# Optimization experiments

Measured on AMD Instinct MI355X. Metric: run time of the kernel, lower is better.

## Reference

```python
import jax, jax.numpy as jnp
import numpy as np

B, S, D = 16, 2048, 128


def setup_inputs() -> dict:
    key = jax.random.key(0)
    kq, kk, kv, km = jax.random.split(key, 4)
    q = jax.random.normal(kq, (B, S, D), dtype=jnp.float32)
    k = jax.random.normal(kk, (B, S, D), dtype=jnp.float32)
    v = jax.random.normal(kv, (B, S, D), dtype=jnp.float32)
    mask = jax.random.randint(km, (B, S, S), 0, 2, dtype=jnp.int32)
    return {"q": q, "k": k, "v": v, "mask": mask}


def softmax_one(x):
    # repo's softmax_one: subtract max, denominator is 1 + sum(exp)
    x = x - jnp.max(x, axis=-1, keepdims=True)
    e = jnp.exp(x)
    return e / (1.0 + jnp.sum(e, axis=-1, keepdims=True))


def reference(q, k, v, mask):
    d_k = k.shape[-1]
    zero = jnp.zeros((q.shape[0], 1, d_k), dtype=q.dtype)
    # prepend zero 'sink' key/value token along the sequence axis
    k1 = jnp.concatenate([zero, k], axis=1)          # [B, S+1, D]
    v1 = jnp.concatenate([zero, v], axis=1)          # [B, S+1, D]
    scores = jnp.einsum('bqd,bkd->bqk', q, k1) / np.sqrt(d_k)  # [B, S, S+1]
    # F.pad(mask, (1, 0)) pads sink column with 0 -> sink score masked
    m = jnp.pad(mask, ((0, 0), (0, 0), (1, 0)))
    scores = jnp.where(m == 0, jnp.float32(-1e9), scores)
    p_attn = softmax_one(scores)                     # [B, S, S+1]
    out = jnp.einsum('bqk,bkd->bqd', p_attn, v1)     # [B, S, D]
    return (out, p_attn)
```

## Files before the change

### kernel.cpp

```cpp
#include <hip/hip_runtime.h>
#include <hip/hip_bf16.h>

typedef __attribute__((ext_vector_type(8))) __bf16 bf16x8;
typedef __attribute__((ext_vector_type(4))) __bf16 bf16x4;
typedef __attribute__((ext_vector_type(4))) float  f32x4;
typedef float f32x4u __attribute__((ext_vector_type(4), aligned(4)));

#define NB 16
#define NS 2048
#define ND 128
#define QT 64
#define KT 64
#define NKT (NS / KT)
#define SCALE 0.08838834764831845f

__device__ __forceinline__ bf16x8 ld8_256(const __bf16* base, int row, int byteInRow) {
    int off = row * 256 + (byteInRow ^ ((row & 7) << 4));
    return *reinterpret_cast<const bf16x8*>(reinterpret_cast<const char*>(base) + off);
}
__device__ __forceinline__ bf16x8 ld8_128(const __bf16* base, int row, int byteInRow) {
    int off = row * 128 + (byteInRow ^ ((row & 7) << 4));
    return *reinterpret_cast<const bf16x8*>(reinterpret_cast<const char*>(base) + off);
}
__device__ __forceinline__ void glds16(const void* g, void* l) {
    __builtin_amdgcn_global_load_lds(
        (const __attribute__((address_space(1))) unsigned int*)g,
        (__attribute__((address_space(3))) unsigned int*)l, 16, 0, 0);
}

__global__ __launch_bounds__(256) void conv_qk(const float* __restrict__ q,
                                               const float* __restrict__ k,
                                               __bf16* __restrict__ qb,
                                               __bf16* __restrict__ kb) {
    size_t i = (size_t)blockIdx.x * 256 + threadIdx.x;
    const float4* qs = (const float4*)q;
    const float4* ks = (const float4*)k;
    float4 a = qs[2 * i], b = qs[2 * i + 1];
    bf16x8 o;
    o[0] = (__bf16)(a.x * SCALE); o[1] = (__bf16)(a.y * SCALE);
    o[2] = (__bf16)(a.z * SCALE); o[3] = (__bf16)(a.w * SCALE);
    o[4] = (__bf16)(b.x * SCALE); o[5] = (__bf16)(b.y * SCALE);
    o[6] = (__bf16)(b.z * SCALE); o[7] = (__bf16)(b.w * SCALE);
    *(bf16x8*)&qb[i * 8] = o;
    a = ks[2 * i]; b = ks[2 * i + 1];
    o[0] = (__bf16)a.x; o[1] = (__bf16)a.y; o[2] = (__bf16)a.z; o[3] = (__bf16)a.w;
    o[4] = (__bf16)b.x; o[5] = (__bf16)b.y; o[6] = (__bf16)b.z; o[7] = (__bf16)b.w;
    *(bf16x8*)&kb[i * 8] = o;
}

__global__ __launch_bounds__(256) void conv_vt(const float* __restrict__ v,
                                               __bf16* __restrict__ vt) {
    int b = blockIdx.x >> 4, st = blockIdx.x & 15;
    int s0 = st * 128, t = threadIdx.x;
    #pragma unroll
    for (int i = 0; i < 8; ++i) {
        int task = i * 256 + t;
        int d = task & 127, sg = task >> 7;
        bf16x8 o;
        #pragma unroll
        for (int j = 0; j < 8; ++j)
            o[j] = (__bf16)v[((size_t)b * NS + s0 + sg * 8 + j) * ND + d];
        *(bf16x8*)&vt[((size_t)b * ND + d) * NS + s0 + sg * 8] = o;
    }
}

__global__ __launch_bounds__(256, 2) void qa_main(
    const __bf16* __restrict__ qb, const __bf16* __restrict__ kb,
    const __bf16* __restrict__ vtb, const int* __restrict__ mg,
    float* __restrict__ outg, float* __restrict__ pg)
{
    __shared__ __align__(16) char bufs[3][KT * ND * 2];
    __shared__ unsigned int bm[QT * 68];
    __shared__ __align__(16) __bf16 Ps[4][16 * KT];

    const int bid = blockIdx.x;
    const int lb  = (bid & 7) * 64 + (bid >> 3);
    const int b   = lb >> 5;
    const int q0  = (lb & 31) * QT;
    const int t   = threadIdx.x;
    const int w   = t >> 6;
    const int l   = t & 63;
    const int l15 = l & 15;
    const int g   = l >> 4;

    const __bf16* kbB  = kb  + (size_t)b * NS * ND;
    const __bf16* vtbB = vtb + (size_t)b * ND * NS;

    #pragma unroll 2
    for (int i = 0; i < 32; ++i) {
        int task = i * 2 + (l >> 5);
        (void)task;
        break;
    }
    for (int i = 0; i < 128; ++i) {
        int row = w * 16 + (i >> 3), chunk = i & 7;
        const int4* mp = (const int4*)(mg + (size_t)(b * NS + q0 + row) * NS + chunk * 256) + l;
        int4 mv = *mp;
        unsigned long long b0 = __ballot(mv.x != 0);
        unsigned long long b1 = __ballot(mv.y != 0);
        unsigned long long b2 = __ballot(mv.z != 0);
        unsigned long long b3 = __ballot(mv.w != 0);
        if (l == 0) {
            uint4 lo = { (unsigned)b0, (unsigned)b1, (unsigned)b2, (unsigned)b3 };
            uint4 hi = { (unsigned)(b0 >> 32), (unsigned)(b1 >> 32),
                         (unsigned)(b2 >> 32), (unsigned)(b3 >> 32) };
            *(uint4*)&bm[row * 68 + chunk * 8]     = lo;
            *(uint4*)&bm[row * 68 + chunk * 8 + 4] = hi;
        }
    }

    if (t < QT) pg[(size_t)(b * NS + q0 + t) * (size_t)(NS + 1)] = 0.0f;

    bf16x8 qf[4];
    {
        const __bf16* qrow = qb + (size_t)(b * NS + q0 + w * 16 + l15) * ND;
        #pragma unroll
        for (int kc = 0; kc < 4; ++kc)
            qf[kc] = *(const bf16x8*)(qrow + kc * 32 + g * 8);
    }

    auto stageK = [&](char* buf, int k0) {
        #pragma unroll
        for (int i = 0; i < 4; ++i) {
            int c = i * 256 + t;
            int row = c >> 4, pc = c & 15, lc = pc ^ (row & 7);
            glds16(kbB + (size_t)(k0 + row) * ND + lc * 8, buf + c * 16);
        }
    };
    auto stageV = [&](char* buf, int k0) {
        #pragma unroll
        for (int i = 0; i < 4; ++i) {
            int c = i * 256 + t;
            int d = c >> 3, pc = c & 7, lc = pc ^ (d & 7);
            glds16(vtbB + (size_t)d * NS + k0 + lc * 8, buf + c * 16);
        }
    };

    stageK(bufs[0], 0);
    __syncthreads();

    const int myrow = w * 16 + l15;
    float mrun = -1e9f, srun = 0.0f;

    for (int kt = 0; kt < NKT; ++kt) {
        const int k0 = kt * KT;
        if (kt + 1 < NKT) stageK(bufs[(kt + 1) & 1], k0 + KT);
        const __bf16* Kbuf = (const __bf16*)bufs[kt & 1];

        f32x4 acc[4];
        #pragma unroll
        for (int c = 0; c < 4; ++c) {
            f32x4 z = {0.f, 0.f, 0.f, 0.f}; acc[c] = z;
            #pragma unroll
            for (int kc = 0; kc < 4; ++kc) {
                bf16x8 kf = ld8_256(Kbuf, c * 16 + l15, kc * 64 + g * 16);
                acc[c] = __builtin_amdgcn_mfma_f32_16x16x32_bf16(kf, qf[kc], acc[c], 0, 0, 0);
            }
        }

        uint4 W = *(const uint4*)&bm[myrow * 68 + (k0 >> 8) * 8 + ((k0 & 128) >> 5)];
        unsigned Wr[4] = { W.x, W.y, W.z, W.w };
        const int sh = ((k0 & 64) >> 2) + g;

        float sv[16], tmax = -1e30f;
        #pragma unroll
        for (int c = 0; c < 4; ++c)
            #pragma unroll
            for (int r = 0; r < 4; ++r) {
                float s = ((Wr[r] >> (sh + c * 4)) & 1u) ? acc[c][r] : -1e30f;
                sv[c * 4 + r] = s;
                tmax = fmaxf(tmax, s);
            }
        tmax = fmaxf(tmax, __shfl_xor(tmax, 16));
        tmax = fmaxf(tmax, __shfl_xor(tmax, 32));
        float mnew = fmaxf(mrun, tmax);
        float corr = __expf(mrun - mnew);
        float ps = 0.f;
        #pragma unroll
        for (int i = 0; i < 16; ++i) ps += __expf(sv[i] - mnew);
        ps += __shfl_xor(ps, 16);
        ps += __shfl_xor(ps, 32);
        srun = srun * corr + ps;
        mrun = mnew;
        __syncthreads();
    }

    const float inv = 1.0f / (1.0f + srun);

    f32x4 oacc[8];
    #pragma unroll
    for (int cf = 0; cf < 8; ++cf) { f32x4 z = {0.f,0.f,0.f,0.f}; oacc[cf] = z; }

    stageK(bufs[0], 0);
    stageV(bufs[1], 0);
    __syncthreads();

    int iA = 0, iB = 1, iC = 2;
    const size_t prow = (size_t)(b * NS + q0 + myrow) * (size_t)(NS + 1);
    __bf16* Psw = Ps[w];

    for (int kt = 0; kt < NKT; ++kt) {
        const int k0 = kt * KT;
        if (kt + 1 < NKT) stageK(bufs[iC], k0 + KT);
        const __bf16* Kbuf = (const __bf16*)bufs[iA];

        f32x4 acc[4];
        #pragma unroll
        for (int c = 0; c < 4; ++c) {
            f32x4 z = {0.f, 0.f, 0.f, 0.f}; acc[c] = z;
            #pragma unroll
            for (int kc = 0; kc < 4; ++kc) {
                bf16x8 kf = ld8_256(Kbuf, c * 16 + l15, kc * 64 + g * 16);
                acc[c] = __builtin_amdgcn_mfma_f32_16x16x32_bf16(kf, qf[kc], acc[c], 0, 0, 0);
            }
        }

        uint4 W = *(const uint4*)&bm[myrow * 68 + (k0 >> 8) * 8 + ((k0 & 128) >> 5)];
        unsigned Wr[4] = { W.x, W.y, W.z, W.w };
        const int sh = ((k0 & 64) >> 2) + g;

        #pragma unroll
        for (int c = 0; c < 4; ++c) {
            f32x4 pv;
            bf16x4 pb;
            #pragma unroll
            for (int r = 0; r < 4; ++r) {
                bool on = (Wr[r] >> (sh + c * 4)) & 1u;
                float p = on ? __expf(acc[c][r] - mrun) * inv : 0.0f;
                pv[r] = p;
                pb[r] = (__bf16)p;
            }
            *(f32x4u*)&pg[prow + 1 + k0 + c * 16 + g * 4] = pv;
            int off = l15 * 128 + ((c * 32 + g * 8) ^ ((l15 & 7) << 4));
            *(bf16x4*)((char*)Psw + off) = pb;
        }

        __syncthreads();
        if (kt + 1 < NKT) stageV(bufs[iA], k0 + KT);
        const __bf16* Vbuf = (const __bf16*)bufs[iB];

        #pragma unroll
        for (int kc = 0; kc < 2; ++kc) {
            bf16x8 af = ld8_128(Psw, l15, kc * 64 + g * 16);
            #pragma unroll
            for (int cf = 0; cf < 8; ++cf) {
                bf16x8 vf = ld8_128(Vbuf, cf * 16 + l15, kc * 64 + g * 16);
                oacc[cf] = __builtin_amdgcn_mfma_f32_16x16x32_bf16(af, vf, oacc[cf], 0, 0, 0);
            }
        }
        __syncthreads();
        int tmp = iA; iA = iC; iC = iB; iB = tmp;
    }

    #pragma unroll
    for (int cf = 0; cf < 8; ++cf)
        #pragma unroll
        for (int r = 0; r < 4; ++r)
            outg[(size_t)(b * NS + q0 + w * 16 + g * 4 + r) * ND + cf * 16 + l15] = oacc[cf][r];
}

__device__ __forceinline__ void stage_rm(__bf16* dst, const float* src, int t) {
    int row = t >> 2, cg = t & 3;
    const float4* s4 = reinterpret_cast<const float4*>(src + (size_t)row * ND) + cg * 8;
    #pragma unroll
    for (int j = 0; j < 8; ++j) {
        float4 f = s4[j];
        bf16x4 h;
        h[0] = (__bf16)f.x; h[1] = (__bf16)f.y; h[2] = (__bf16)f.z; h[3] = (__bf16)f.w;
        int off = (cg * 64 + j * 8) ^ ((row & 7) << 4);
        *reinterpret_cast<bf16x4*>(reinterpret_cast<char*>(dst) + row * 256 + off) = h;
    }
}

__global__ __launch_bounds__(256, 2) void qa_fused_fb(
    const float* __restrict__ qg, const float* __restrict__ kg,
    const float* __restrict__ vg, const int* __restrict__ mg,
    float* __restrict__ outg, float* __restrict__ pg)
{
    __shared__ __bf16 Qs[QT * ND];
    __shared__ __bf16 Ks[KT * ND];
    __shared__ __bf16 Vt[ND * KT];
    __shared__ __bf16 Psf[4 * 16 * KT];
    __shared__ unsigned int bmf[QT][64];

    const int bid = blockIdx.x;
    const int lb  = (bid & 7) * 64 + (bid >> 3);
    const int b   = lb >> 5;
    const int q0  = (lb & 31) * QT;
    const int t   = threadIdx.x;
    const int w   = t >> 6;
    const int l   = t & 63;
    const int l15 = l & 15;
    const int g   = l >> 4;

    stage_rm(Qs, qg + ((size_t)b * NS + q0) * ND, t);
    if (t < QT) pg[((size_t)b * NS + q0 + t) * (size_t)(NS + 1)] = 0.0f;
    __syncthreads();

    bf16x8 qf[4];
    const int arow = w * 16 + l15;
    #pragma unroll
    for (int kc = 0; kc < 4; ++kc) qf[kc] = ld8_256(Qs, arow, kc * 64 + g * 16);

    float mrun[4], srun[4];
    #pragma unroll
    for (int r = 0; r < 4; ++r) { mrun[r] = -1e9f; srun[r] = 0.0f; }

    for (int kt = 0; kt < NKT; ++kt) {
        const int k0 = kt * KT;
        __syncthreads();
        stage_rm(Ks, kg + ((size_t)b * NS + k0) * ND, t);
        #pragma unroll 4
        for (int i = 0; i < 16; ++i) {
            int row = w * 16 + i;
            int mv = mg[((size_t)b * NS + (q0 + row)) * NS + k0 + l];
            unsigned long long bal = __ballot(mv != 0);
            if (l == 0) {
                bmf[row][2 * kt]     = (unsigned)bal;
                bmf[row][2 * kt + 1] = (unsigned)(bal >> 32);
            }
        }
        __syncthreads();

        f32x4 acc[4];
        #pragma unroll
        for (int c = 0; c < 4; ++c) {
            f32x4 z = {0.f, 0.f, 0.f, 0.f};
            acc[c] = z;
            #pragma unroll
            for (int kc = 0; kc < 4; ++kc) {
                bf16x8 bf = ld8_256(Ks, c * 16 + l15, kc * 64 + g * 16);
                acc[c] = __builtin_amdgcn_mfma_f32_16x16x32_bf16(qf[kc], bf, acc[c], 0, 0, 0);
            }
        }

        #pragma unroll
        for (int r = 0; r < 4; ++r) {
            const int row = w * 16 + g * 4 + r;
            const unsigned w0 = bmf[row][2 * kt], w1 = bmf[row][2 * kt + 1];
            float sv[4], tmax = -1e9f;
            #pragma unroll
            for (int c = 0; c < 4; ++c) {
                int cb = c * 16 + l15;
                unsigned word = (c < 2) ? w0 : w1;
                bool on = (word >> (cb & 31)) & 1u;
                float s = on ? acc[c][r] * SCALE : -1e9f;
                sv[c] = s;
                tmax = fmaxf(tmax, s);
            }
            #pragma unroll
            for (int d = 1; d < 16; d <<= 1) tmax = fmaxf(tmax, __shfl_xor(tmax, d));
            float mnew = fmaxf(mrun[r], tmax);
            float corr = __expf(mrun[r] - mnew);
            float ps = 0.f;
            #pragma unroll
            for (int c = 0; c < 4; ++c) ps += __expf(sv[c] - mnew);
            #pragma unroll
            for (int d = 1; d < 16; d <<= 1) ps += __shfl_xor(ps, d);
            srun[r] = srun[r] * corr + ps;
            mrun[r] = mnew;
        }
    }

    float inv[4];
    #pragma unroll
    for (int r = 0; r < 4; ++r) inv[r] = 1.0f / (1.0f + srun[r]);

    f32x4 oacc[8];
    #pragma unroll
    for (int cf = 0; cf < 8; ++cf) { f32x4 z = {0.f,0.f,0.f,0.f}; oacc[cf] = z; }

    __bf16* Psw = Psf + w * (16 * KT);

    for (int kt = 0; kt < NKT; ++kt) {
        const int k0 = kt * KT;
        __syncthreads();
        stage_rm(Ks, kg + ((size_t)b * NS + k0) * ND, t);
        {
            int kk = t >> 2, dg = t & 3;
            const float4* s4 = reinterpret_cast<const float4*>(vg + ((size_t)b * NS + k0 + kk) * ND) + dg * 8;
            #pragma unroll
            for (int j = 0; j < 8; ++j) {
                float4 f = s4[j];
                int d0 = dg * 32 + j * 4;
                float fv[4] = {f.x, f.y, f.z, f.w};
                #pragma unroll
                for (int e = 0; e < 4; ++e) {
                    int d = d0 + e;
                    int off = d * 128 + ((kk * 2) ^ ((d & 7) << 4));
                    *reinterpret_cast<__bf16*>(reinterpret_cast<char*>(Vt) + off) = (__bf16)fv[e];
                }
            }
        }
        __syncthreads();

        f32x4 acc[4];
        #pragma unroll
        for (int c = 0; c < 4; ++c) {
            f32x4 z = {0.f, 0.f, 0.f, 0.f};
            acc[c] = z;
            #pragma unroll
            for (int kc = 0; kc < 4; ++kc) {
                bf16x8 bf = ld8_256(Ks, c * 16 + l15, kc * 64 + g * 16);
                acc[c] = __builtin_amdgcn_mfma_f32_16x16x32_bf16(qf[kc], bf, acc[c], 0, 0, 0);
            }
        }

        #pragma unroll
        for (int r = 0; r < 4; ++r) {
            const int row16 = g * 4 + r;
            const int row = w * 16 + row16;
            const unsigned w0 = bmf[row][2 * kt], w1 = bmf[row][2 * kt + 1];
            const size_t prow = ((size_t)b * NS + q0 + row) * (size_t)(NS + 1);
            #pragma unroll
            for (int c = 0; c < 4; ++c) {
                int cb = c * 16 + l15;
                unsigned word = (c < 2) ? w0 : w1;
                bool on = (word >> (cb & 31)) & 1u;
                float p = on ? __expf(acc[c][r] * SCALE - mrun[r]) * inv[r] : 0.0f;
                pg[prow + 1 + k0 + cb] = p;
                int off = row16 * 128 + ((cb * 2) ^ ((row16 & 7) << 4));
                *reinterpret_cast<__bf16*>(reinterpret_cast<char*>(Psw) + off) = (__bf16)p;
            }
        }

        #pragma unroll
        for (int kc = 0; kc < 2; ++kc) {
            bf16x8 af = ld8_128(Psw, l15, kc * 64 + g * 16);
            #pragma unroll
            for (int cf = 0; cf < 8; ++cf) {
                bf16x8 vf = ld8_128(Vt, cf * 16 + l15, kc * 64 + g * 16);
                oacc[cf] = __builtin_amdgcn_mfma_f32_16x16x32_bf16(af, vf, oacc[cf], 0, 0, 0);
            }
        }
    }

    #pragma unroll
    for (int cf = 0; cf < 8; ++cf)
        #pragma unroll
        for (int r = 0; r < 4; ++r)
            outg[((size_t)b * NS + q0 + w * 16 + g * 4 + r) * ND + cf * 16 + l15] = oacc[cf][r];
}

extern "C" void kernel_launch(void* const* d_in, const int* in_sizes, int n_in,
                              void* d_out, int out_size, void* d_ws, size_t ws_size,
                              hipStream_t stream) {
    const float* q = (const float*)d_in[0];
    const float* k = (const float*)d_in[1];
    const float* v = (const float*)d_in[2];
    const int*  mk = (const int*)d_in[3];
    float* out = (float*)d_out;
    float* p   = out + (size_t)NB * NS * ND;

    const size_t elems = (size_t)NB * NS * ND;
    const size_t need  = elems * 2 * 3;

    if (ws_size >= need) {
        __bf16* qb = (__bf16*)d_ws;
        __bf16* kb = qb + elems;
        __bf16* vt = kb + elems;
        conv_qk<<<dim3((unsigned)(elems / 8 / 256)), dim3(256), 0, stream>>>(q, k, qb, kb);
        conv_vt<<<dim3(NB * 16), dim3(256), 0, stream>>>(v, vt);
        qa_main<<<dim3(NB * (NS / QT)), dim3(256), 0, stream>>>(qb, kb, vt, mk, out, p);
    } else {
        qa_fused_fb<<<dim3(NB * (NS / QT)), dim3(256), 0, stream>>>(q, k, v, mk, out, p);
    }
}
```

Measured before the change: 665.3 us.

## Load K/V fragments directly to registers and stream mask per tile

The main kernel stops staging K and V tiles through LDS with global_load_lds and instead loads MFMA fragments straight from global memory into registers, prefetching the next tile while computing the current one, which removes most __syncthreads. The upfront full-row mask ballot pass is replaced by per-tile int4 mask loads during the first pass, which store compact 16-bit per-lane masks in LDS for reuse in the second pass. The V transpose kernel now goes through an LDS tile so its global accesses are coalesced. In exchange, register pressure rises, and each wave re-fetches K/V from global/L2 with no sharing through LDS.

```diff
diff --git a/kernel.cpp b/kernel.cpp
--- a/kernel.cpp
+++ b/kernel.cpp
@@ -21,11 +21,6 @@
 __device__ __forceinline__ bf16x8 ld8_128(const __bf16* base, int row, int byteInRow) {
     int off = row * 128 + (byteInRow ^ ((row & 7) << 4));
     return *reinterpret_cast<const bf16x8*>(reinterpret_cast<const char*>(base) + off);
-}
-__device__ __forceinline__ void glds16(const void* g, void* l) {
-    __builtin_amdgcn_global_load_lds(
-        (const __attribute__((address_space(1))) unsigned int*)g,
-        (__attribute__((address_space(3))) unsigned int*)l, 16, 0, 0);
 }
 
 __global__ __launch_bounds__(256) void conv_qk(const float* __restrict__ q,
@@ -50,17 +45,27 @@
 
 __global__ __launch_bounds__(256) void conv_vt(const float* __restrict__ v,
                                                __bf16* __restrict__ vt) {
-    int b = blockIdx.x >> 4, st = blockIdx.x & 15;
-    int s0 = st * 128, t = threadIdx.x;
-    #pragma unroll
-    for (int i = 0; i < 8; ++i) {
-        int task = i * 256 + t;
-        int d = task & 127, sg = task >> 7;
-        bf16x8 o;
-        #pragma unroll
-        for (int j = 0; j < 8; ++j)
-            o[j] = (__bf16)v[((size_t)b * NS + s0 + sg * 8 + j) * ND + d];
-        *(bf16x8*)&vt[((size_t)b * ND + d) * NS + s0 + sg * 8] = o;
+    __shared__ __bf16 tile[128 * 128];
+    const int b = blockIdx.x >> 4, st = blockIdx.x & 15;
+    const int s0 = st * 128, t = threadIdx.x;
+    const int rlane = t >> 5, cv = (t & 31) * 4;
+    #pragma unroll
+    for (int it = 0; it < 16; ++it) {
+        int s = rlane + it * 8;
+        float4 f = *(const float4*)(v + ((size_t)b * NS + s0 + s) * ND + cv);
+        bf16x4 h;
+        h[0] = (__bf16)f.x; h[1] = (__bf16)f.y; h[2] = (__bf16)f.z; h[3] = (__bf16)f.w;
+        *(bf16x4*)&tile[s * 128 + (cv ^ (s & 60))] = h;
+    }
+    __syncthreads();
+    #pragma unroll
+    for (int it = 0; it < 16; ++it) {
+        int d = rlane + it * 8;
+        bf16x4 o;
+        #pragma unroll
+        for (int e = 0; e < 4; ++e)
+            o[e] = tile[(cv + e) * 128 + (d ^ ((cv + e) & 60))];
+        *(bf16x4*)&vt[((size_t)b * ND + d) * NS + s0 + cv] = o;
     }
 }
 
@@ -69,8 +74,7 @@
     const __bf16* __restrict__ vtb, const int* __restrict__ mg,
     float* __restrict__ outg, float* __restrict__ pg)
 {
-    __shared__ __align__(16) char bufs[3][KT * ND * 2];
-    __shared__ unsigned int bm[QT * 68];
+    __shared__ unsigned short bmt[NKT * 256];
     __shared__ __align__(16) __bf16 Ps[4][16 * KT];
 
     const int bid = blockIdx.x;
@@ -82,174 +86,144 @@
     const int l   = t & 63;
     const int l15 = l & 15;
     const int g   = l >> 4;
+    const int myrow = w * 16 + l15;
 
     const __bf16* kbB  = kb  + (size_t)b * NS * ND;
     const __bf16* vtbB = vtb + (size_t)b * ND * NS;
-
-    #pragma unroll 2
-    for (int i = 0; i < 32; ++i) {
-        int task = i * 2 + (l >> 5);
-        (void)task;
-        break;
-    }
-    for (int i = 0; i < 128; ++i) {
-        int row = w * 16 + (i >> 3), chunk = i & 7;
-        const int4* mp = (const int4*)(mg + (size_t)(b * NS + q0 + row) * NS + chunk * 256) + l;
-        int4 mv = *mp;
-        unsigned long long b0 = __ballot(mv.x != 0);
-        unsigned long long b1 = __ballot(mv.y != 0);
-        unsigned long long b2 = __ballot(mv.z != 0);
-        unsigned long long b3 = __ballot(mv.w != 0);
-        if (l == 0) {
-            uint4 lo = { (unsigned)b0, (unsigned)b1, (unsigned)b2, (unsigned)b3 };
-            uint4 hi = { (unsigned)(b0 >> 32), (unsigned)(b1 >> 32),
-                         (unsigned)(b2 >> 32), (unsigned)(b3 >> 32) };
-            *(uint4*)&bm[row * 68 + chunk * 8]     = lo;
-            *(uint4*)&bm[row * 68 + chunk * 8 + 4] = hi;
-        }
-    }
+    const int*    mrow = mg  + (size_t)(b * NS + q0 + myrow) * NS;
 
     if (t < QT) pg[(size_t)(b * NS + q0 + t) * (size_t)(NS + 1)] = 0.0f;
 
     bf16x8 qf[4];
     {
-        const __bf16* qrow = qb + (size_t)(b * NS + q0 + w * 16 + l15) * ND;
+        const __bf16* qrow = qb + (size_t)(b * NS + q0 + myrow) * ND;
         #pragma unroll
         for (int kc = 0; kc < 4; ++kc)
             qf[kc] = *(const bf16x8*)(qrow + kc * 32 + g * 8);
     }
 
-    auto stageK = [&](char* buf, int k0) {
-        #pragma unroll
-        for (int i = 0; i < 4; ++i) {
-            int c = i * 256 + t;
-            int row = c >> 4, pc = c & 15, lc = pc ^ (row & 7);
-            glds16(kbB + (size_t)(k0 + row) * ND + lc * 8, buf + c * 16);
-        }
+    bf16x8 kf[16];
+    f32x4  acc[4];
+
+    auto loadK = [&](int k0) {
+        #pragma unroll
+        for (int c = 0; c < 4; ++c)
+            #pragma unroll
+            for (int kc = 0; kc < 4; ++kc)
+                kf[c * 4 + kc] = *(const bf16x8*)(kbB + (size_t)(k0 + c * 16 + l15) * ND + kc * 32 + g * 8);
     };
-    auto stageV = [&](char* buf, int k0) {
-        #pragma unroll
-        for (int i = 0; i < 4; ++i) {
-            int c = i * 256 + t;
-            int d = c >> 3, pc = c & 7, lc = pc ^ (d & 7);
-            glds16(vtbB + (size_t)d * NS + k0 + lc * 8, buf + c * 16);
+    auto qk = [&]() {
+        #pragma unroll
+        for (int c = 0; c < 4; ++c) {
+            f32x4 z = {0.f, 0.f, 0.f, 0.f}; acc[c] = z;
+            #pragma unroll
+            for (int kc = 0; kc < 4; ++kc)
+                acc[c] = __builtin_amdgcn_mfma_f32_16x16x32_bf16(kf[c * 4 + kc], qf[kc], acc[c], 0, 0, 0);
         }
     };
 
-    stageK(bufs[0], 0);
-    __syncthreads();
-
-    const int myrow = w * 16 + l15;
     float mrun = -1e9f, srun = 0.0f;
+    int4 mA[4], mB[4];
+
+    auto stepA = [&](int kt, const int4* mcur, int4* mnxt) {
+        qk();
+        const int kn = kt + 1;
+        if (kn < NKT) {
+            loadK(kn * KT);
+            #pragma unroll
+            for (int c = 0; c < 4; ++c)
+                mnxt[c] = *(const int4*)(mrow + kn * KT + c * 16 + g * 4);
+        }
+        float sv[16]; unsigned bits = 0;
+        #pragma unroll
+        for (int c = 0; c < 4; ++c) {
+            int mm[4] = {mcur[c].x, mcur[c].y, mcur[c].z, mcur[c].w};
+            #pragma unroll
+            for (int r = 0; r < 4; ++r) {
+                bool on = mm[r] != 0;
+                sv[c * 4 + r] = on ? acc[c][r] : -1e30f;
+                bits |= on ? (1u << (c * 4 + r)) : 0u;
+            }
+        }
+        float x0 = fmaxf(fmaxf(sv[0], sv[1]),  fmaxf(sv[2], sv[3]));
+        float x1 = fmaxf(fmaxf(sv[4], sv[5]),  fmaxf(sv[6], sv[7]));
+        float x2 = fmaxf(fmaxf(sv[8], sv[9]),  fmaxf(sv[10], sv[11]));
+        float x3 = fmaxf(fmaxf(sv[12], sv[13]), fmaxf(sv[14], sv[15]));
+        float mx = fmaxf(fmaxf(x0, x1), fmaxf(x2, x3));
+        mx = fmaxf(mx, __shfl_xor(mx, 16));
+        mx = fmaxf(mx, __shfl_xor(mx, 32));
+        float mnew = fmaxf(mrun, mx);
+        float e[16];
+        #pragma unroll
+        for (int i = 0; i < 16; ++i) e[i] = __expf(sv[i] - mnew);
+        float s0 = (e[0] + e[1]) + (e[2] + e[3]);
+        float s1 = (e[4] + e[5]) + (e[6] + e[7]);
+        float s2 = (e[8] + e[9]) + (e[10] + e[11]);
+        float s3 = (e[12] + e[13]) + (e[14] + e[15]);
+        float ps = (s0 + s1) + (s2 + s3);
+        ps += __shfl_xor(ps, 16);
+        ps += __shfl_xor(ps, 32);
+        srun = srun * __expf(mrun - mnew) + ps;
+        mrun = mnew;
+        bmt[kt * 256 + t] = (unsigned short)bits;
+    };
+
+    loadK(0);
+    #pragma unroll
+    for (int c = 0; c < 4; ++c) mA[c] = *(const int4*)(mrow + c * 16 + g * 4);
+    for (int kt = 0; kt < NKT; kt += 2) {
+        stepA(kt,     mA, mB);
+        stepA(kt + 1, mB, mA);
+    }
+
+    const float inv = 1.0f / (1.0f + srun);
+
+    f32x4 oacc[8];
+    #pragma unroll
+    for (int cf = 0; cf < 8; ++cf) { f32x4 z = {0.f, 0.f, 0.f, 0.f}; oacc[cf] = z; }
+
+    bf16x8 vf[16];
+    auto loadV = [&](int k0) {
+        #pragma unroll
+        for (int kc = 0; kc < 2; ++kc)
+            #pragma unroll
+            for (int cf = 0; cf < 8; ++cf)
+                vf[kc * 8 + cf] = *(const bf16x8*)(vtbB + (size_t)(cf * 16 + l15) * NS + k0 + kc * 32 + g * 8);
+    };
+
+    loadK(0);
+    loadV(0);
+    const size_t prow = (size_t)(b * NS + q0 + myrow) * (size_t)(NS + 1);
+    __bf16* Psw = Ps[w];
 
     for (int kt = 0; kt < NKT; ++kt) {
         const int k0 = kt * KT;
-        if (kt + 1 < NKT) stageK(bufs[(kt + 1) & 1], k0 + KT);
-        const __bf16* Kbuf = (const __bf16*)bufs[kt & 1];
-
-        f32x4 acc[4];
+        qk();
+        if (kt + 1 < NKT) loadK(k0 + KT);
+
+        unsigned bits = bmt[kt * 256 + t];
         #pragma unroll
         for (int c = 0; c < 4; ++c) {
-            f32x4 z = {0.f, 0.f, 0.f, 0.f}; acc[c] = z;
-            #pragma unroll
-            for (int kc = 0; kc < 4; ++kc) {
-                bf16x8 kf = ld8_256(Kbuf, c * 16 + l15, kc * 64 + g * 16);
-                acc[c] = __builtin_amdgcn_mfma_f32_16x16x32_bf16(kf, qf[kc], acc[c], 0, 0, 0);
-            }
-        }
-
-        uint4 W = *(const uint4*)&bm[myrow * 68 + (k0 >> 8) * 8 + ((k0 & 128) >> 5)];
-        unsigned Wr[4] = { W.x, W.y, W.z, W.w };
-        const int sh = ((k0 & 64) >> 2) + g;
-
-        float sv[16], tmax = -1e30f;
-        #pragma unroll
-        for (int c = 0; c < 4; ++c)
+            f32x4 pv; bf16x4 pb;
             #pragma unroll
             for (int r = 0; r < 4; ++r) {
-                float s = ((Wr[r] >> (sh + c * 4)) & 1u) ? acc[c][r] : -1e30f;
-                sv[c * 4 + r] = s;
-                tmax = fmaxf(tmax, s);
-            }
-        tmax = fmaxf(tmax, __shfl_xor(tmax, 16));
-        tmax = fmaxf(tmax, __shfl_xor(tmax, 32));
-        float mnew = fmaxf(mrun, tmax);
-        float corr = __expf(mrun - mnew);
-        float ps = 0.f;
-        #pragma unroll
-        for (int i = 0; i < 16; ++i) ps += __expf(sv[i] - mnew);
-        ps += __shfl_xor(ps, 16);
-        ps += __shfl_xor(ps, 32);
-        srun = srun * corr + ps;
-        mrun = mnew;
-        __syncthreads();
-    }
-
-    const float inv = 1.0f / (1.0f + srun);
-
-    f32x4 oacc[8];
-    #pragma unroll
-    for (int cf = 0; cf < 8; ++cf) { f32x4 z = {0.f,0.f,0.f,0.f}; oacc[cf] = z; }
-
-    stageK(bufs[0], 0);
-    stageV(bufs[1], 0);
-    __syncthreads();
-
-    int iA = 0, iB = 1, iC = 2;
-    const size_t prow = (size_t)(b * NS + q0 + myrow) * (size_t)(NS + 1);
-    __bf16* Psw = Ps[w];
-
-    for (int kt = 0; kt < NKT; ++kt) {
-        const int k0 = kt * KT;
-        if (kt + 1 < NKT) stageK(bufs[iC], k0 + KT);
-        const __bf16* Kbuf = (const __bf16*)bufs[iA];
-
-        f32x4 acc[4];
-        #pragma unroll
-        for (int c = 0; c < 4; ++c) {
-            f32x4 z = {0.f, 0.f, 0.f, 0.f}; acc[c] = z;
-            #pragma unroll
-            for (int kc = 0; kc < 4; ++kc) {
-                bf16x8 kf = ld8_256(Kbuf, c * 16 + l15, kc * 64 + g * 16);
-                acc[c] = __builtin_amdgcn_mfma_f32_16x16x32_bf16(kf, qf[kc], acc[c], 0, 0, 0);
-            }
-        }
-
-        uint4 W = *(const uint4*)&bm[myrow * 68 + (k0 >> 8) * 8 + ((k0 & 128) >> 5)];
-        unsigned Wr[4] = { W.x, W.y, W.z, W.w };
-        const int sh = ((k0 & 64) >> 2) + g;
-
-        #pragma unroll
-        for (int c = 0; c < 4; ++c) {
-            f32x4 pv;
-            bf16x4 pb;
-            #pragma unroll
-            for (int r = 0; r < 4; ++r) {
-                bool on = (Wr[r] >> (sh + c * 4)) & 1u;
+                bool on = (bits >> (c * 4 + r)) & 1u;
                 float p = on ? __expf(acc[c][r] - mrun) * inv : 0.0f;
-                pv[r] = p;
-                pb[r] = (__bf16)p;
+                pv[r] = p; pb[r] = (__bf16)p;
             }
             *(f32x4u*)&pg[prow + 1 + k0 + c * 16 + g * 4] = pv;
             int off = l15 * 128 + ((c * 32 + g * 8) ^ ((l15 & 7) << 4));
             *(bf16x4*)((char*)Psw + off) = pb;
         }
 
-        __syncthreads();
-        if (kt + 1 < NKT) stageV(bufs[iA], k0 + KT);
-        const __bf16* Vbuf = (const __bf16*)bufs[iB];
-
         #pragma unroll
         for (int kc = 0; kc < 2; ++kc) {
             bf16x8 af = ld8_128(Psw, l15, kc * 64 + g * 16);
             #pragma unroll
-            for (int cf = 0; cf < 8; ++cf) {
-                bf16x8 vf = ld8_128(Vbuf, cf * 16 + l15, kc * 64 + g * 16);
-                oacc[cf] = __builtin_amdgcn_mfma_f32_16x16x32_bf16(af, vf, oacc[cf], 0, 0, 0);
-            }
-        }
-        __syncthreads();
-        int tmp = iA; iA = iC; iC = iB; iB = tmp;
+            for (int cf = 0; cf < 8; ++cf)
+                oacc[cf] = __builtin_amdgcn_mfma_f32_16x16x32_bf16(af, vf[kc * 8 + cf], oacc[cf], 0, 0, 0);
+        }
+        if (kt + 1 < NKT) loadV(k0 + KT);
     }
 
     #pragma unroll
@@ -411,14 +385,14 @@
             const int row16 = g * 4 + r;
             const int row = w * 16 + row16;
             const unsigned w0 = bmf[row][2 * kt], w1 = bmf[row][2 * kt + 1];
-            const size_t prow = ((size_t)b * NS + q0 + row) * (size_t)(NS + 1);
+            const size_t prowf = ((size_t)b * NS + q0 + row) * (size_t)(NS + 1);
             #pragma unroll
             for (int c = 0; c < 4; ++c) {
                 int cb = c * 16 + l15;
                 unsigned word = (c < 2) ? w0 : w1;
                 bool on = (word >> (cb & 31)) & 1u;
                 float p = on ? __expf(acc[c][r] * SCALE - mrun[r]) * inv[r] : 0.0f;
-                pg[prow + 1 + k0 + cb] = p;
+                pg[prowf + 1 + k0 + cb] = p;
                 int off = row16 * 128 + ((cb * 2) ^ ((row16 & 7) << 4));
                 *reinterpret_cast<__bf16*>(reinterpret_cast<char*>(Psw) + off) = (__bf16)p;
             }
@@ -429,8 +403,8 @@
             bf16x8 af = ld8_128(Psw, l15, kc * 64 + g * 16);
             #pragma unroll
             for (int cf = 0; cf < 8; ++cf) {
-                bf16x8 vf = ld8_128(Vt, cf * 16 + l15, kc * 64 + g * 16);
-                oacc[cf] = __builtin_amdgcn_mfma_f32_16x16x32_bf16(af, vf, oacc[cf], 0, 0, 0);
+                bf16x8 vfr = ld8_128(Vt, cf * 16 + l15, kc * 64 + g * 16);
+                oacc[cf] = __builtin_amdgcn_mfma_f32_16x16x32_bf16(af, vfr, oacc[cf], 0, 0, 0);
             }
         }
     }
```

Measured after the change: 778.3 us. +17.0%, slower.
